# Kernel optimization log

Hardware: AMD Instinct MI355X
Metric: run time of the kernel (lower is better)

Reference implementation:

```python
import jax, jax.numpy as jnp
import numpy as np

EMBED_DIM = 1024
NUM_HEADS = 16
HEAD_DIM = EMBED_DIM // NUM_HEADS


def setup_inputs() -> dict:
    key = jax.random.key(0)
    ks = jax.random.split(key, 9)
    s = 1.0 / np.sqrt(EMBED_DIM)
    inp = {"x": jax.random.normal(ks[0], (2, 2048, EMBED_DIM), dtype=jnp.float32)}
    for i, name in enumerate(["q", "k", "v", "out"]):
        inp[f"W_{name}"] = jax.random.uniform(ks[1 + 2 * i], (EMBED_DIM, EMBED_DIM), jnp.float32, -s, s)
        inp[f"b_{name}"] = jax.random.uniform(ks[2 + 2 * i], (EMBED_DIM,), jnp.float32, -s, s)
    return inp


def _heads(x):
    # [B, S, D] -> [B, H, S, Dh]
    b, s, _ = x.shape
    return x.reshape(b, s, NUM_HEADS, HEAD_DIM).transpose(0, 2, 1, 3)


def reference(x, W_q, b_q, W_k, b_k, W_v, b_v, W_out, b_out):
    q = _heads(x @ W_q.T + b_q)
    k = _heads(x @ W_k.T + b_k)
    v = _heads(x @ W_v.T + b_v)
    scale = HEAD_DIM ** 0.5
    logits = jnp.einsum("bhqd,bhkd->bhqk", q, k) / scale  # [B,H,S,S]
    s = x.shape[1]
    causal = jnp.tril(jnp.ones((s, s), dtype=bool))
    logits = jnp.where(causal, logits, -jnp.inf)
    a = jax.nn.softmax(logits, axis=-1)
    o = jnp.einsum("bhqk,bhkd->bhqd", a, v)
    o = o.transpose(0, 2, 1, 3).reshape(x.shape[0], s, EMBED_DIM)
    return o @ W_out.T + b_out
```

## Files before the change

### kernel.cpp

```cpp
#include <hip/hip_runtime.h>
#include <hip/hip_bf16.h>

typedef __bf16 bf16_t;
typedef __bf16 bf16x8 __attribute__((ext_vector_type(8)));
typedef __bf16 bf16x4 __attribute__((ext_vector_type(4)));
typedef float  f32x4  __attribute__((ext_vector_type(4)));

#define MFMA16(a, b, c) __builtin_amdgcn_mfma_f32_16x16x32_bf16((a), (b), (c), 0, 0, 0)

constexpr int E  = 1024;
constexpr int S  = 2048;
constexpr int H  = 16;
constexpr int M  = 4096;

__device__ __forceinline__ void glds16(const bf16_t* src, bf16_t* dst) {
  __builtin_amdgcn_global_load_lds(
      (const __attribute__((address_space(1))) void*)src,
      (__attribute__((address_space(3))) void*)dst, 16, 0, 0);
}

template <int ROWS, int NT>
__device__ __forceinline__ void stage_tile(const bf16_t* g, int gld,
                                           bf16_t* lds, int tid) {
  const int w = tid >> 6, l = tid & 63;
#pragma unroll
  for (int i = 0; i < ROWS * 8 / NT; ++i) {
    const int c = i * NT + w * 64 + l;
    const int row = c >> 3;
    const int gch = (c & 7) ^ (row & 7);
    glds16(g + (size_t)row * gld + gch * 8, lds + (size_t)(i * NT + w * 64) * 8);
  }
}

__device__ __forceinline__ bf16x8 read_frag(const bf16_t* lds, int row, int kc) {
  return *(const bf16x8*)(lds + (size_t)((row << 3) + (kc ^ (row & 7))) * 8);
}

__global__ void cvt_all_kernel(const float* __restrict__ x,
                               const float* __restrict__ w0, const float* __restrict__ w1,
                               const float* __restrict__ w2, const float* __restrict__ w3,
                               bf16_t* __restrict__ xb,
                               bf16_t* __restrict__ o0, bf16_t* __restrict__ o1,
                               bf16_t* __restrict__ o2, bf16_t* __restrict__ o3) {
  const int bid = blockIdx.x;
  const float* s;
  bf16_t* d;
  int idx;
  if (bid < 4096) {
    s = x; d = xb; idx = bid * 256 + threadIdx.x;
  } else {
    const int seg = (bid - 4096) >> 10;
    s = seg == 0 ? w0 : seg == 1 ? w1 : seg == 2 ? w2 : w3;
    d = seg == 0 ? o0 : seg == 1 ? o1 : seg == 2 ? o2 : o3;
    idx = ((bid - 4096) & 1023) * 256 + threadIdx.x;
  }
  float4 v = ((const float4*)s)[idx];
  bf16x4 o;
  o[0] = (bf16_t)v.x; o[1] = (bf16_t)v.y; o[2] = (bf16_t)v.z; o[3] = (bf16_t)v.w;
  ((bf16x4*)d)[idx] = o;
}

__global__ __launch_bounds__(512, 2) void qkv8_kernel(
    const bf16_t* __restrict__ xb, const bf16_t* __restrict__ W3,
    const float* __restrict__ bq, const float* __restrict__ bk,
    const float* __restrict__ bv, bf16_t* __restrict__ Qb) {
  __shared__ __align__(16) bf16_t As[2][256 * 64];
  __shared__ __align__(16) bf16_t Bs[2][192 * 64];
  const int tid = threadIdx.x;
  const int l = tid & 63, lq = l & 15, qd = l >> 4;
  const int w = tid >> 6, wm = w >> 2, wn = w & 3;

  const int wg = blockIdx.x;
  const int xcd = wg & 7, i5 = wg >> 3;
  const int region = xcd * 2 + (i5 >> 4);
  const int j = i5 & 15;
  const int bx = (region & 3) * 4 + (j & 3);
  const int by = (region >> 2) * 4 + (j >> 2);
  const int m0 = by * 256, n0 = bx * 192;

  const bf16_t* Ag = xb + (size_t)m0 * E;
  const bf16_t* Bg = W3 + (size_t)n0 * E;

  f32x4 acc[8][3];
#pragma unroll
  for (int mi = 0; mi < 8; ++mi)
#pragma unroll
    for (int n = 0; n < 3; ++n) acc[mi][n] = (f32x4){0.f, 0.f, 0.f, 0.f};

  stage_tile<256, 512>(Ag, E, As[0], tid);
  stage_tile<192, 512>(Bg, E, Bs[0], tid);
  asm volatile("s_waitcnt vmcnt(0)" ::: "memory");
  __builtin_amdgcn_s_barrier();

#pragma unroll 1
  for (int g = 0; g < 16; ++g) {
    const int s = g & 1;
    const bf16_t* Al = As[s];
    const bf16_t* Bl = Bs[s];
    bf16_t* An = As[s ^ 1];
    bf16_t* Bn = Bs[s ^ 1];
    const bf16_t* Agn = Ag + (g + 1) * 64;
    const bf16_t* Bgn = Bg + (g + 1) * 64;
    const bool more = (g < 15);
#pragma unroll
    for (int q = 0; q < 4; ++q) {
      const int mh = q >> 1, kk = q & 1;
      bf16x8 af[4], bfr[3];
#pragma unroll
      for (int jj = 0; jj < 4; ++jj)
        af[jj] = read_frag(Al, wm * 128 + (mh * 4 + jj) * 16 + lq, kk * 4 + qd);
#pragma unroll
      for (int n = 0; n < 3; ++n)
        bfr[n] = read_frag(Bl, wn * 48 + n * 16 + lq, kk * 4 + qd);
      if (more) {
        if (q == 0) stage_tile<128, 512>(Agn, E, An, tid);
        else if (q == 1) stage_tile<128, 512>(Agn + (size_t)128 * E, E, An + 128 * 64, tid);
        else if (q == 2) stage_tile<192, 512>(Bgn, E, Bn, tid);
      }
      __builtin_amdgcn_s_barrier();
      asm volatile("s_waitcnt lgkmcnt(0)" ::: "memory");
      __builtin_amdgcn_sched_barrier(0);
      __builtin_amdgcn_s_setprio(1);
#pragma unroll
      for (int jj = 0; jj < 4; ++jj)
#pragma unroll
        for (int n = 0; n < 3; ++n)
          acc[mh * 4 + jj][n] = MFMA16(af[jj], bfr[n], acc[mh * 4 + jj][n]);
      __builtin_amdgcn_s_setprio(0);
      if (q == 3 && more) asm volatile("s_waitcnt vmcnt(0)" ::: "memory");
      __builtin_amdgcn_s_barrier();
    }
  }

#pragma unroll
  for (int n = 0; n < 3; ++n) {
    const int col = n0 + wn * 48 + n * 16 + lq;
    const int mat = col >> 10, cc = col & 1023;
    const float bvv = (mat == 0 ? bq : mat == 1 ? bk : bv)[cc];
    const float sc = (mat == 0) ? 0.18033688011112043f : 1.0f;
    bf16_t* Out = Qb + (size_t)mat * ((size_t)M * E);
#pragma unroll
    for (int mi = 0; mi < 8; ++mi)
#pragma unroll
      for (int r = 0; r < 4; ++r) {
        const int row = m0 + wm * 128 + mi * 16 + qd * 4 + r;
        Out[(size_t)row * E + cc] = (bf16_t)((acc[mi][n][r] + bvv) * sc);
      }
  }
}

__global__ __launch_bounds__(256) void vtrans_kernel(const bf16_t* __restrict__ Vb,
                                                     bf16_t* __restrict__ VT) {
  constexpr int LDT = 72;
  __shared__ __align__(16) bf16_t T[64 * LDT];
  const int tid = threadIdx.x;
  const int st = blockIdx.x, bh = blockIdx.y;
  const int b = bh >> 4, h = bh & 15;
  const int s0 = st * 64;
  const size_t rowbase = (size_t)b * S;
#pragma unroll
  for (int i = 0; i < 2; ++i) {
    const int c = i * 256 + tid;
    const int sl = c >> 3, dp = c & 7;
    const int a = sl >> 4, bb = (sl >> 2) & 3, cc = sl & 3;
    const int p = (a >> 1) * 32 + bb * 8 + (a & 1) * 4 + cc;
    bf16x8 v = *(const bf16x8*)(Vb + (rowbase + s0 + sl) * E + h * 64 + dp * 8);
    *(bf16x8*)&T[p * LDT + dp * 8] = v;
  }
  __syncthreads();
#pragma unroll
  for (int i = 0; i < 2; ++i) {
    const int c = i * 256 + tid;
    const int d = c >> 3, pp = (c & 7) * 8;
    bf16x8 o;
#pragma unroll
    for (int j = 0; j < 8; ++j) o[j] = T[(pp + j) * LDT + d];
    *(bf16x8*)&VT[((size_t)bh * 64 + d) * S + s0 + pp] = o;
  }
}

__global__ __launch_bounds__(256) void oproj_gemm_kernel(
    const bf16_t* __restrict__ Ob, const bf16_t* __restrict__ wo,
    const float* __restrict__ bo, float* __restrict__ out) {
  __shared__ __align__(16) bf16_t As[64 * 64];
  __shared__ __align__(16) bf16_t Bs[128 * 64];
  const int tid = threadIdx.x;
  const int n0 = blockIdx.x * 128;
  const int m0 = blockIdx.y * 64;
  const int w = tid >> 6, l = tid & 63, lq = l & 15, qd = l >> 4;
  const int wr = (w >> 1) * 32, wc = (w & 1) * 64;

  f32x4 acc[2][4];
#pragma unroll
  for (int i = 0; i < 2; ++i)
#pragma unroll
    for (int j = 0; j < 4; ++j) acc[i][j] = (f32x4){0.f, 0.f, 0.f, 0.f};

  for (int kt = 0; kt < 16; ++kt) {
    __syncthreads();
    stage_tile<64, 256>(Ob + (size_t)m0 * E + kt * 64, E, As, tid);
    stage_tile<128, 256>(wo + (size_t)n0 * E + kt * 64, E, Bs, tid);
    __syncthreads();
#pragma unroll
    for (int ks = 0; ks < 2; ++ks) {
      bf16x8 af[2], bw[4];
#pragma unroll
      for (int mi = 0; mi < 2; ++mi)
        af[mi] = read_frag(As, wr + mi * 16 + lq, ks * 4 + qd);
#pragma unroll
      for (int ni = 0; ni < 4; ++ni)
        bw[ni] = read_frag(Bs, wc + ni * 16 + lq, ks * 4 + qd);
#pragma unroll
      for (int mi = 0; mi < 2; ++mi)
#pragma unroll
        for (int ni = 0; ni < 4; ++ni)
          acc[mi][ni] = MFMA16(af[mi], bw[ni], acc[mi][ni]);
    }
  }
#pragma unroll
  for (int ni = 0; ni < 4; ++ni) {
    const int col = n0 + wc + ni * 16 + lq;
    const float bvv = bo[col];
#pragma unroll
    for (int mi = 0; mi < 2; ++mi)
#pragma unroll
      for (int r = 0; r < 4; ++r) {
        const int row = m0 + wr + mi * 16 + qd * 4 + r;
        out[(size_t)row * E + col] = acc[mi][ni][r] + bvv;
      }
  }
}

__global__ __launch_bounds__(256, 2) void attn_kernel(
    const bf16_t* __restrict__ Q, const bf16_t* __restrict__ K,
    const bf16_t* __restrict__ VT, bf16_t* __restrict__ O) {
  __shared__ __align__(16) bf16_t Ks[2][64 * 64];
  __shared__ __align__(16) bf16_t Vt[2][64 * 64];

  const int tid = threadIdx.x;
  const int w = tid >> 6, l = tid & 63;
  const int lq = l & 15, qd = l >> 4;
  const int bid = blockIdx.x;
  const int g = bid & 7, t = bid >> 3;
  const int bh = g * 4 + (t & 3);
  const int p = t >> 2;
  const int b = bh >> 4, h = bh & 15;
  const size_t rowbase = (size_t)b * S;
  const bf16_t* Kg = K + rowbase * E + h * 64;
  const bf16_t* Vg = VT + (size_t)bh * 64 * S;

  stage_tile<64, 256>(Kg, E, Ks[0], tid);
  stage_tile<64, 256>(Vg, S, Vt[0], tid);
  int cb = 0;

#pragma unroll 1
  for (int seg = 0; seg < 2; ++seg) {
    const int qt = seg ? p : 31 - p;
    const int qr = qt * 64 + w * 16;

    bf16x8 aq[2];
#pragma unroll
    for (int ks = 0; ks < 2; ++ks)
      aq[ks] = *(const bf16x8*)(Q + (rowbase + qr + lq) * E + h * 64 +
                                ks * 32 + qd * 8);

    f32x4 oacc[4];
#pragma unroll
    for (int nt = 0; nt < 4; ++nt) oacc[nt] = (f32x4){0.f, 0.f, 0.f, 0.f};
    float rs4[4] = {0.f, 0.f, 0.f, 0.f};

    for (int kt = 0; kt <= qt; ++kt) {
      __syncthreads();
      if (kt < qt) {
        const int kn = (kt + 1) * 64;
        stage_tile<64, 256>(Kg + (size_t)kn * E, E, Ks[cb ^ 1], tid);
        stage_tile<64, 256>(Vg + kn, S, Vt[cb ^ 1], tid);
      } else if (seg == 0) {
        stage_tile<64, 256>(Kg, E, Ks[cb ^ 1], tid);
        stage_tile<64, 256>(Vg, S, Vt[cb ^ 1], tid);
      }
      const bf16_t* Kc = Ks[cb];
      const bf16_t* Vc = Vt[cb];
      const int k0 = kt * 64;
      const bool needmask = (kt == qt);

      f32x4 sacc[4];
#pragma unroll
      for (int nt = 0; nt < 4; ++nt) sacc[nt] = (f32x4){0.f, 0.f, 0.f, 0.f};
#pragma unroll
      for (int ks = 0; ks < 2; ++ks) {
        bf16x8 bk[4];
#pragma unroll
        for (int nt = 0; nt < 4; ++nt)
          bk[nt] = read_frag(Kc, nt * 16 + lq, ks * 4 + qd);
#pragma unroll
        for (int nt = 0; nt < 4; ++nt)
          sacc[nt] = MFMA16(bk[nt], aq[ks], sacc[nt]);
      }
      bf16x8 ap[2];
#pragma unroll
      for (int nt = 0; nt < 4; ++nt)
#pragma unroll
        for (int r = 0; r < 4; ++r) {
          float pv = exp2f(sacc[nt][r]);
          if (needmask) {
            const int kg = k0 + nt * 16 + qd * 4 + r;
            const int qg = qr + lq;
            pv = (kg > qg) ? 0.f : pv;
          }
          rs4[nt] += pv;
          ap[nt >> 1][((nt & 1) << 2) | r] = (bf16_t)pv;
        }
#pragma unroll
      for (int ks = 0; ks < 2; ++ks) {
        bf16x8 bv[4];
#pragma unroll
        for (int nt = 0; nt < 4; ++nt)
          bv[nt] = read_frag(Vc, nt * 16 + lq, ks * 4 + qd);
#pragma unroll
        for (int nt = 0; nt < 4; ++nt)
          oacc[nt] = MFMA16(ap[ks], bv[nt], oacc[nt]);
      }
      cb ^= 1;
    }

    float rs = (rs4[0] + rs4[1]) + (rs4[2] + rs4[3]);
    rs += __shfl_xor(rs, 16);
    rs += __shfl_xor(rs, 32);
    float rinv[4];
#pragma unroll
    for (int r = 0; r < 4; ++r) rinv[r] = 1.0f / __shfl(rs, qd * 4 + r);
#pragma unroll
    for (int nt = 0; nt < 4; ++nt)
#pragma unroll
      for (int r = 0; r < 4; ++r) {
        const int qg = qr + qd * 4 + r;
        O[(rowbase + qg) * E + h * 64 + nt * 16 + lq] =
            (bf16_t)(oacc[nt][r] * rinv[r]);
      }
  }
}

extern "C" void kernel_launch(void* const* d_in, const int* in_sizes, int n_in,
                              void* d_out, int out_size, void* d_ws, size_t ws_size,
                              hipStream_t stream) {
  const float* x  = (const float*)d_in[0];
  const float* Wq = (const float*)d_in[1];
  const float* bq = (const float*)d_in[2];
  const float* Wk = (const float*)d_in[3];
  const float* bk = (const float*)d_in[4];
  const float* Wv = (const float*)d_in[5];
  const float* bv = (const float*)d_in[6];
  const float* Wo = (const float*)d_in[7];
  const float* bo = (const float*)d_in[8];
  float* out = (float*)d_out;

  unsigned char* ws = (unsigned char*)d_ws;
  constexpr size_t MB = 1ull << 20;
  bf16_t* xb  = (bf16_t*)(ws + 0 * MB);
  bf16_t* wqb = (bf16_t*)(ws + 8 * MB);
  bf16_t* wkb = (bf16_t*)(ws + 10 * MB);
  bf16_t* wvb = (bf16_t*)(ws + 12 * MB);
  bf16_t* wob = (bf16_t*)(ws + 14 * MB);
  bf16_t* Qb  = (bf16_t*)(ws + 16 * MB);
  bf16_t* Kb  = (bf16_t*)(ws + 24 * MB);
  bf16_t* Vb  = (bf16_t*)(ws + 32 * MB);
  bf16_t* VT  = (bf16_t*)(ws + 40 * MB);
  bf16_t* Ob  = xb;

  cvt_all_kernel<<<4096 + 4 * 1024, 256, 0, stream>>>(
      x, Wq, Wk, Wv, Wo, xb, wqb, wkb, wvb, wob);

  qkv8_kernel<<<256, 512, 0, stream>>>(xb, wqb, bq, bk, bv, Qb);

  vtrans_kernel<<<dim3(32, 32), 256, 0, stream>>>(Vb, VT);

  attn_kernel<<<512, 256, 0, stream>>>(Qb, Kb, VT, Ob);

  oproj_gemm_kernel<<<dim3(8, 64), 256, 0, stream>>>(Ob, wob, bo, out);
}
```

Before: 183.4 us.

## Software-pipeline PV matmul behind next QK tile with triple-buffered V

Restructures the attention inner loop so the P·V MFMAs for the previous key tile are issued right after the current tile's QK^T MFMAs, with V triple-buffered in LDS so the deferred tile stays resident. The aim is to overlap the exp/softmax VALU work with matrix-core work. It also replaces the scalar row-sum and shuffle reduction with an extra MFMA against a ones vector, uses the hardware exp2 builtin, and raises wave priority around the MFMA section. In exchange it adds 8 KB of LDS, one extra MFMA per k-step and more live registers, which could lower occupancy.

```diff
diff --git a/kernel.cpp b/kernel.cpp
--- a/kernel.cpp
+++ b/kernel.cpp
@@ -235,7 +235,7 @@
     const bf16_t* __restrict__ Q, const bf16_t* __restrict__ K,
     const bf16_t* __restrict__ VT, bf16_t* __restrict__ O) {
   __shared__ __align__(16) bf16_t Ks[2][64 * 64];
-  __shared__ __align__(16) bf16_t Vt[2][64 * 64];
+  __shared__ __align__(16) bf16_t Vt[3][64 * 64];
 
   const int tid = threadIdx.x;
   const int w = tid >> 6, l = tid & 63;
@@ -249,9 +249,14 @@
   const bf16_t* Kg = K + rowbase * E + h * 64;
   const bf16_t* Vg = VT + (size_t)bh * 64 * S;
 
+  bf16x8 ones;
+#pragma unroll
+  for (int j = 0; j < 8; ++j) ones[j] = (bf16_t)1.0f;
+
   stage_tile<64, 256>(Kg, E, Ks[0], tid);
   stage_tile<64, 256>(Vg, S, Vt[0], tid);
   int cb = 0;
+  int vcur = 0;
 
 #pragma unroll 1
   for (int seg = 0; seg < 2; ++seg) {
@@ -267,26 +272,43 @@
     f32x4 oacc[4];
 #pragma unroll
     for (int nt = 0; nt < 4; ++nt) oacc[nt] = (f32x4){0.f, 0.f, 0.f, 0.f};
-    float rs4[4] = {0.f, 0.f, 0.f, 0.f};
+    f32x4 osum = (f32x4){0.f, 0.f, 0.f, 0.f};
+    bf16x8 ap_prev[2];
+    int vprev = vcur;
+
+    auto do_pv = [&](const bf16_t* Vp) {
+#pragma unroll
+      for (int ks = 0; ks < 2; ++ks) {
+        bf16x8 bv[4];
+#pragma unroll
+        for (int nt = 0; nt < 4; ++nt)
+          bv[nt] = read_frag(Vp, nt * 16 + lq, ks * 4 + qd);
+#pragma unroll
+        for (int nt = 0; nt < 4; ++nt)
+          oacc[nt] = MFMA16(ap_prev[ks], bv[nt], oacc[nt]);
+        osum = MFMA16(ap_prev[ks], ones, osum);
+      }
+    };
 
     for (int kt = 0; kt <= qt; ++kt) {
       __syncthreads();
+      const int vnext = (vcur + 1 == 3) ? 0 : vcur + 1;
       if (kt < qt) {
         const int kn = (kt + 1) * 64;
         stage_tile<64, 256>(Kg + (size_t)kn * E, E, Ks[cb ^ 1], tid);
-        stage_tile<64, 256>(Vg + kn, S, Vt[cb ^ 1], tid);
+        stage_tile<64, 256>(Vg + kn, S, Vt[vnext], tid);
       } else if (seg == 0) {
         stage_tile<64, 256>(Kg, E, Ks[cb ^ 1], tid);
-        stage_tile<64, 256>(Vg, S, Vt[cb ^ 1], tid);
+        stage_tile<64, 256>(Vg, S, Vt[vnext], tid);
       }
       const bf16_t* Kc = Ks[cb];
-      const bf16_t* Vc = Vt[cb];
       const int k0 = kt * 64;
       const bool needmask = (kt == qt);
 
       f32x4 sacc[4];
 #pragma unroll
       for (int nt = 0; nt < 4; ++nt) sacc[nt] = (f32x4){0.f, 0.f, 0.f, 0.f};
+      __builtin_amdgcn_s_setprio(1);
 #pragma unroll
       for (int ks = 0; ks < 2; ++ks) {
         bf16x8 bk[4];
@@ -297,39 +319,30 @@
         for (int nt = 0; nt < 4; ++nt)
           sacc[nt] = MFMA16(bk[nt], aq[ks], sacc[nt]);
       }
-      bf16x8 ap[2];
+      if (kt > 0) do_pv(Vt[vprev]);
+      __builtin_amdgcn_s_setprio(0);
+
 #pragma unroll
       for (int nt = 0; nt < 4; ++nt)
 #pragma unroll
         for (int r = 0; r < 4; ++r) {
-          float pv = exp2f(sacc[nt][r]);
+          float pv = __builtin_amdgcn_exp2f(sacc[nt][r]);
           if (needmask) {
             const int kg = k0 + nt * 16 + qd * 4 + r;
             const int qg = qr + lq;
             pv = (kg > qg) ? 0.f : pv;
           }
-          rs4[nt] += pv;
-          ap[nt >> 1][((nt & 1) << 2) | r] = (bf16_t)pv;
+          ap_prev[nt >> 1][((nt & 1) << 2) | r] = (bf16_t)pv;
         }
-#pragma unroll
-      for (int ks = 0; ks < 2; ++ks) {
-        bf16x8 bv[4];
-#pragma unroll
-        for (int nt = 0; nt < 4; ++nt)
-          bv[nt] = read_frag(Vc, nt * 16 + lq, ks * 4 + qd);
-#pragma unroll
-        for (int nt = 0; nt < 4; ++nt)
-          oacc[nt] = MFMA16(ap[ks], bv[nt], oacc[nt]);
-      }
+      vprev = vcur;
+      vcur = vnext;
       cb ^= 1;
     }
-
-    float rs = (rs4[0] + rs4[1]) + (rs4[2] + rs4[3]);
-    rs += __shfl_xor(rs, 16);
-    rs += __shfl_xor(rs, 32);
+    do_pv(Vt[vprev]);
+
     float rinv[4];
 #pragma unroll
-    for (int r = 0; r < 4; ++r) rinv[r] = 1.0f / __shfl(rs, qd * 4 + r);
+    for (int r = 0; r < 4; ++r) rinv[r] = 1.0f / osum[r];
 #pragma unroll
     for (int nt = 0; nt < 4; ++nt)
 #pragma unroll
```

Result: no change. 180.6 us (-1.5%).
